# Performance work log

Measured on AMD Instinct MI355X. Metric: run time of the kernel, lower is better.

The kernel has to match this reference:

```python
import jax, jax.numpy as jnp
import numpy as np

N, H, P, NB, IN, E, B = 10000, 64, 12, 3, 3, 160000, 2
EPS = 1e-5


def _ln(x, w, b):
    # LayerNorm over last two dims [N, H] with affine params [N, H]
    mu = jnp.mean(x, axis=(-2, -1), keepdims=True)
    var = jnp.mean((x - mu) ** 2, axis=(-2, -1), keepdims=True)
    return (x - mu) * jax.lax.rsqrt(var + EPS) * w + b


def _proj(x, w1, b1, w2, b2):
    h = jax.nn.relu(jnp.einsum('...i,oi->...o', x, w1) + b1)
    return jnp.einsum('...i,oi->...o', h, w2) + b2


def setup_inputs() -> dict:
    key = jax.random.key(0)
    ks = jax.random.split(key, 24)
    s = lambda k, shape, fan: jax.random.normal(k, shape, jnp.float32) * (1.0 / np.sqrt(fan))
    inp = {
        'x': jax.random.normal(ks[0], (B, P, N, IN), jnp.float32),
        'edge_index': jax.random.randint(ks[1], (2, E), 0, N, jnp.int64),
        'pos': jax.random.normal(ks[2], (N, H), jnp.float32),
        # input projection (IN -> H -> H)
        'iw1': s(ks[3], (H, IN), IN), 'ib1': jnp.zeros((H,), jnp.float32),
        'iw2': s(ks[4], (H, H), H), 'ib2': jnp.zeros((H,), jnp.float32),
        # pos projection (H -> H -> H)
        'pw1': s(ks[5], (H, H), H), 'pb1': jnp.zeros((H,), jnp.float32),
        'pw2': s(ks[6], (H, H), H), 'pb2': jnp.zeros((H,), jnp.float32),
        # attention over skip connections [NB+1, 1]
        'attn': jax.random.normal(ks[7], (NB + 1, 1), jnp.float32),
        # per-block params, stacked on leading NB axis
        'gnw': jnp.ones((NB, N, H), jnp.float32), 'gnb': jnp.zeros((NB, N, H), jnp.float32),
        'tnw': jnp.ones((NB, N, H), jnp.float32), 'tnb': jnp.zeros((NB, N, H), jnp.float32),
        'tcw': s(ks[8], (NB, P, P), P), 'tcb': jnp.zeros((NB, P), jnp.float32),
        # output projection (H -> H -> H)
        'ow1': s(ks[9], (H, H), H), 'ob1': jnp.zeros((H,), jnp.float32),
        'ow2': s(ks[10], (H, H), H), 'ob2': jnp.zeros((H,), jnp.float32),
    }
    return inp


def reference(x, edge_index, pos, iw1, ib1, iw2, ib2, pw1, pb1, pw2, pb2,
              attn, gnw, gnb, tnw, tnb, tcw, tcb, ow1, ob1, ow2, ob2):
    row, col = edge_index[0], edge_index[1]
    # LGConv gcn_norm (no self loops): deg from target index, sym normalization
    deg = jax.ops.segment_sum(jnp.ones((E,), x.dtype), col, num_segments=N)
    dis = jnp.where(deg > 0, jax.lax.rsqrt(jnp.maximum(deg, 1.0)) * (deg > 0), 0.0)
    dis = jnp.where(deg > 0, deg ** -0.5, 0.0)
    norm = dis[row] * dis[col]  # [E]

    x = _proj(x, iw1, ib1, iw2, ib2)            # [B,P,N,H]
    x = x + _proj(pos, pw1, pb1, pw2, pb2)       # broadcast [N,H]

    skip = [x]
    for i in range(NB):
        x = _ln(x, gnw[i], gnb[i])
        # LightGCN propagate: out[col] += norm * x[row]
        msg = norm[:, None] * x[:, :, row, :]    # [B,P,E,H]
        x = jnp.zeros_like(x).at[:, :, col, :].add(msg)
        x = _ln(x, tnw[i], tnb[i])
        # 1x1 Conv2d over the period/channel axis
        x = jnp.einsum('qp,bpnh->bqnh', tcw[i], x) + tcb[i][None, :, None, None]
        skip.append(x)

    a = jax.nn.softmax(attn, axis=0)[:, 0]       # [NB+1]
    x = sum(s * a[k] for k, s in enumerate(skip))
    return _proj(x, ow1, ob1, ow2, ob2)
```

## Files before the change

### kernel.cpp

```cpp
#include <hip/hip_runtime.h>
#include <stdint.h>

constexpr int N_ = 10000, H_ = 64, P_ = 12, NB_ = 3, IN_ = 3, E_ = 160000, B_ = 2;
constexpr int S_  = B_ * P_;
constexpr int NH_ = N_ * H_;
constexpr int BPS_ = N_ / 4;
constexpr int NB64_ = (N_ + 63) / 64;
constexpr int NPAIR_ = S_ / 2;
constexpr int PROPNB_ = N_ / 8;
constexpr int PROPBLK_ = NPAIR_ * PROPNB_;
constexpr int PROPPX_  = PROPBLK_ / 8;
constexpr int EPAD_ = E_ + N_;
constexpr float EPS_ = 1e-5f;

#define DEVFN __device__ __forceinline__

DEVFN float softmax4(const float* a, int k) {
    float m = fmaxf(fmaxf(a[0], a[1]), fmaxf(a[2], a[3]));
    float e0 = __expf(a[0] - m), e1 = __expf(a[1] - m);
    float e2 = __expf(a[2] - m), e3 = __expf(a[3] - m);
    float s = e0 + e1 + e2 + e3;
    float ek = (k == 0 ? e0 : k == 1 ? e1 : k == 2 ? e2 : e3);
    return ek / s;
}

DEVFN float wred(float v) {
#pragma unroll
    for (int d = 32; d; d >>= 1) v += __shfl_xor(v, d, 64);
    return v;
}

DEVFN void fma4(float m, const float4& a, float4& acc) {
    acc.x = fmaf(m, a.x, acc.x); acc.y = fmaf(m, a.y, acc.y);
    acc.z = fmaf(m, a.z, acc.z); acc.w = fmaf(m, a.w, acc.w);
}

DEVFN void xred4(float4& a) {
    a.x += __shfl_xor(a.x, 16, 64); a.y += __shfl_xor(a.y, 16, 64);
    a.z += __shfl_xor(a.z, 16, 64); a.w += __shfl_xor(a.w, 16, 64);
    a.x += __shfl_xor(a.x, 32, 64); a.y += __shfl_xor(a.y, 32, 64);
    a.z += __shfl_xor(a.z, 32, 64); a.w += __shfl_xor(a.w, 32, 64);
}

DEVFN void stage_swz(const float4* __restrict__ src, float* __restrict__ dst, int t) {
    for (int f = t; f < 1024; f += 256) {
        int r = f >> 4, c4 = f & 15;
        float4 v = src[f];
        *(float4*)&dst[r * 64 + ((c4 ^ (r >> 2)) << 2)] = v;
    }
}

DEVFN void stage_swz_guard(const float4* __restrict__ src, float* __restrict__ dst,
                           int t, int nvalid) {
    for (int f = t; f < 1024; f += 256) {
        int r = f >> 4, c4 = f & 15;
        float4 v = make_float4(0.f, 0.f, 0.f, 0.f);
        if (r < nvalid) v = src[f];
        *(float4*)&dst[r * 64 + ((c4 ^ (r >> 2)) << 2)] = v;
    }
}

DEVFN void gemm64(const float* __restrict__ As, const float* __restrict__ Bs,
                  int tn4, int to4, float ov[4][4]) {
    const float* arow = As + tn4 * 64;
    const float* brow = Bs + to4 * 64;
#pragma unroll 4
    for (int j4 = 0; j4 < 16; ++j4) {
        int ca = (j4 << 2) ^ tn4;
        int cb = (j4 << 2) ^ to4;
        float4 a[4], b[4];
#pragma unroll
        for (int i = 0; i < 4; ++i) a[i] = *(const float4*)&arow[i * 64 + ca];
#pragma unroll
        for (int k = 0; k < 4; ++k) b[k] = *(const float4*)&brow[k * 64 + cb];
#pragma unroll
        for (int i = 0; i < 4; ++i)
#pragma unroll
            for (int k = 0; k < 4; ++k) {
                ov[i][k] = fmaf(a[i].x, b[k].x, ov[i][k]);
                ov[i][k] = fmaf(a[i].y, b[k].y, ov[i][k]);
                ov[i][k] = fmaf(a[i].z, b[k].z, ov[i][k]);
                ov[i][k] = fmaf(a[i].w, b[k].w, ov[i][k]);
            }
    }
}

__global__ void k_deg(const int* __restrict__ ei, int* __restrict__ deg) {
    int e = blockIdx.x * 256 + threadIdx.x;
    if (e < E_) atomicAdd(&deg[ei[E_ + e]], 1);
}

__global__ void k_scan(const int* __restrict__ deg, int* __restrict__ offs,
                       int* __restrict__ cursor, float* __restrict__ dis) {
    __shared__ int part[1024];
    int t = threadIdx.x;
    int base = t * 10;
    int cnt = 0;
    for (int k = 0; k < 10; k++) {
        int i = base + k;
        if (i < N_) cnt += (deg[i] + 1) & ~1;
    }
    part[t] = cnt;
    __syncthreads();
    for (int d = 1; d < 1024; d <<= 1) {
        int v = 0;
        if (t >= d) v = part[t - d];
        __syncthreads();
        if (t >= d) part[t] += v;
        __syncthreads();
    }
    int run = (t > 0) ? part[t - 1] : 0;
    for (int k = 0; k < 10; k++) {
        int i = base + k;
        if (i < N_) {
            offs[i] = run; cursor[i] = run;
            int dg = deg[i];
            dis[i] = dg > 0 ? rsqrtf((float)dg) : 0.f;
            run += (dg + 1) & ~1;
        }
    }
    if (t == 1023) offs[N_] = part[1023];
}

__global__ void k_scatter(const int* __restrict__ ei, const float* __restrict__ dis,
                          int* __restrict__ cursor, int2* __restrict__ csr_pack) {
    int e = blockIdx.x * 256 + threadIdx.x;
    if (e >= E_) return;
    int r = ei[e], c = ei[E_ + e];
    float nm = dis[r] * dis[c];
    int p = atomicAdd(&cursor[c], 1);
    csr_pack[p] = make_int2(r << 4, __float_as_int(nm));
}

__global__ void k_red(const float2* __restrict__ part, float* __restrict__ st, int count) {
    __shared__ float rsm[4], rsq[4];
    int s = blockIdx.x, t = threadIdx.x, w = t >> 6, lane = t & 63;
    float sm = 0.f, sq = 0.f;
    for (int k = t; k < count; k += 256) {
        float2 p = part[s * BPS_ + k];
        sm += p.x; sq += p.y;
    }
    sm = wred(sm); sq = wred(sq);
    if (lane == 0) { rsm[w] = sm; rsq[w] = sq; }
    __syncthreads();
    if (t == 0) {
        st[s * 2]     = rsm[0] + rsm[1] + rsm[2] + rsm[3];
        st[s * 2 + 1] = rsq[0] + rsq[1] + rsq[2] + rsq[3];
    }
}

__global__ void k_wb(const int* __restrict__ offs, const int2* __restrict__ csr_pack,
                     const float* __restrict__ gw, const float* __restrict__ gb,
                     float* __restrict__ Wt, float* __restrict__ Bt) {
    int t = threadIdx.x;
    int w = t >> 6, lane = t & 63;
    int sub = lane >> 4, hl = lane & 15;
    int n = blockIdx.x * 4 + w;
    const float4* W4 = (const float4*)gw;
    const float4* B4 = (const float4*)gb;
    int e0 = offs[n], e1 = offs[n + 1];
    float4 AW = make_float4(0, 0, 0, 0), AB = make_float4(0, 0, 0, 0);
    for (int e = e0 + sub * 2; e < e1; e += 8) {
        int4 mp = *(const int4*)&csr_pack[e];
        float m0 = __int_as_float(mp.y), m1 = __int_as_float(mp.w);
        int i0 = mp.x + hl, i1 = mp.z + hl;
        float4 a = W4[i0], b = W4[i1], c = B4[i0], d = B4[i1];
        fma4(m0, a, AW); fma4(m1, b, AW);
        fma4(m0, c, AB); fma4(m1, d, AB);
    }
    xred4(AW); xred4(AB);
    if (sub == 0) {
        ((float4*)Wt)[n * 16 + hl] = AW;
        ((float4*)Bt)[n * 16 + hl] = AB;
    }
}

__global__ void k_posproj(const float* __restrict__ pos, const float* __restrict__ w1,
                          const float* __restrict__ b1, const float* __restrict__ w2,
                          const float* __restrict__ b2, float* __restrict__ out) {
    __shared__ float w1T[64 * 65], w2T[64 * 65];
    __shared__ float stage[4][64];
    int t = threadIdx.x;
    for (int k = t; k < 4096; k += 256) {
        int o = k >> 6, j = k & 63;
        w1T[j * 65 + o] = w1[k];
        w2T[j * 65 + o] = w2[k];
    }
    __syncthreads();
    int w = t >> 6, lane = t & 63;
    int n = blockIdx.x * 4 + w;
    float v = pos[n * 64 + lane];
    stage[w][lane] = v;
    float h = b1[lane];
#pragma unroll
    for (int j = 0; j < 64; j++) h = fmaf(w1T[j * 65 + lane], stage[w][j], h);
    h = fmaxf(h, 0.f);
    stage[w][lane] = h;
    float o2 = b2[lane];
#pragma unroll
    for (int j = 0; j < 64; j++) o2 = fmaf(w2T[j * 65 + lane], stage[w][j], o2);
    out[n * 64 + lane] = o2;
}

__global__ void k_in(const float* __restrict__ xin, const float* __restrict__ iw1,
                     const float* __restrict__ ib1, const float* __restrict__ iw2,
                     const float* __restrict__ ib2, const float* __restrict__ pp,
                     const float* __restrict__ attn, const float* __restrict__ gw0,
                     float* __restrict__ xw, float* __restrict__ acc,
                     float2* __restrict__ part) {
    __shared__ __align__(16) float U[4096];
    __shared__ __align__(16) float B2s[4096];
    __shared__ float xin_s[192], iw1_s[192], bias1[64], bias2[64];
    __shared__ float rsm[4], rsq[4], sa0s;
    int t = threadIdx.x;
    int blk = blockIdx.x;
    int s = blk / NB64_, bn = blk % NB64_;
    int n0 = bn * 64;
    int nvalid = min(64, N_ - n0);
    stage_swz((const float4*)iw2, B2s, t);
    if (t < 192) {
        iw1_s[t] = iw1[t];
        int n = n0 + t / 3;
        xin_s[t] = (n < N_) ? xin[(size_t)s * (N_ * 3) + n0 * 3 + t] : 0.f;
    }
    if (t < 64) { bias1[t] = ib1[t]; bias2[t] = ib2[t]; }
    if (t == 0) sa0s = softmax4(attn, 0);
    __syncthreads();
    int tn = t >> 4, to = t & 15;
    int tn4 = tn << 2, to4 = to << 2;
    float h1[4][4];
#pragma unroll
    for (int i = 0; i < 4; i++) {
        float a0 = xin_s[(tn4 + i) * 3], a1 = xin_s[(tn4 + i) * 3 + 1],
              a2 = xin_s[(tn4 + i) * 3 + 2];
#pragma unroll
        for (int k = 0; k < 4; k++) {
            int o = to4 + k;
            float h = bias1[o];
            h = fmaf(iw1_s[o * 3], a0, h);
            h = fmaf(iw1_s[o * 3 + 1], a1, h);
            h = fmaf(iw1_s[o * 3 + 2], a2, h);
            h1[i][k] = fmaxf(h, 0.f);
        }
    }
#pragma unroll
    for (int i = 0; i < 4; i++)
        *(float4*)&U[(tn4 + i) * 64 + (to4 ^ tn4)] =
            make_float4(h1[i][0], h1[i][1], h1[i][2], h1[i][3]);
    __syncthreads();
    float ov[4][4];
#pragma unroll
    for (int i = 0; i < 4; i++)
#pragma unroll
        for (int k = 0; k < 4; k++) ov[i][k] = bias2[to4 + k];
    gemm64(U, B2s, tn4, to4, ov);
    __syncthreads();
#pragma unroll
    for (int i = 0; i < 4; i++)
        *(float4*)&U[(tn4 + i) * 64 + to4] =
            make_float4(ov[i][0], ov[i][1], ov[i][2], ov[i][3]);
    __syncthreads();
    const float4* pp4 = (const float4*)pp + n0 * 16;
    const float4* gw4 = (const float4*)gw0 + n0 * 16;
    float4* xw4 = (float4*)xw + (size_t)s * (NH_ / 4) + n0 * 16;
    float4* ac4 = (float4*)acc + (size_t)s * (NH_ / 4) + n0 * 16;
    float sa0 = sa0s;
    float sm = 0.f, sq = 0.f;
    for (int f = t; f < 1024; f += 256) {
        int r = f >> 4;
        if (r < nvalid) {
            float4 v = ((const float4*)U)[f];
            float4 p = pp4[f];
            v.x += p.x; v.y += p.y; v.z += p.z; v.w += p.w;
            float4 a;
            a.x = sa0 * v.x; a.y = sa0 * v.y; a.z = sa0 * v.z; a.w = sa0 * v.w;
            ac4[f] = a;
            sm += v.x + v.y + v.z + v.w;
            sq += v.x * v.x + v.y * v.y + v.z * v.z + v.w * v.w;
            float4 g = gw4[f];
            v.x *= g.x; v.y *= g.y; v.z *= g.z; v.w *= g.w;
            xw4[f] = v;
        }
    }
    int w = t >> 6, lane = t & 63;
    sm = wred(sm); sq = wred(sq);
    if (lane == 0) { rsm[w] = sm; rsq[w] = sq; }
    __syncthreads();
    if (t == 0) {
        float2 pr;
        pr.x = rsm[0] + rsm[1] + rsm[2] + rsm[3];
        pr.y = rsq[0] + rsq[1] + rsq[2] + rsq[3];
        part[s * BPS_ + bn] = pr;
    }
}

__global__ void k_prop(const float* __restrict__ xw, const int* __restrict__ offs,
                       const int2* __restrict__ csr_pack, const float* __restrict__ Wt,
                       const float* __restrict__ Bt, const float* __restrict__ st,
                       float* __restrict__ y, float2* __restrict__ part) {
    __shared__ float bs[4][2][4];
    int t = threadIdx.x;
    int w = t >> 6, lane = t & 63;
    int nsel = lane >> 5;
    int str  = (lane >> 4) & 1;
    int hl   = lane & 15;
    int orig = blockIdx.x;
    int gw = (orig & 7) * PROPPX_ + (orig >> 3);
    int pr = gw / PROPNB_;
    int blkin = gw % PROPNB_;
    int n = blkin * 8 + w * 2 + nsel;
    int s0 = pr * 2;
    const float4* xh0 = (const float4*)(xw + (size_t)s0 * NH_) + hl;
    const float4* xh1 = xh0 + (NH_ / 4);
    int e0 = offs[n], e1 = offs[n + 1];
    float4 A0 = make_float4(0, 0, 0, 0), A1 = make_float4(0, 0, 0, 0);
    int e = e0 + str * 2;
    while (__any(e < e1)) {
        if (e < e1) {
            int4 mp = *(const int4*)&csr_pack[e];
            float m0 = __int_as_float(mp.y), m1 = __int_as_float(mp.w);
            float4 a = xh0[mp.x], b = xh0[mp.z];
            float4 c = xh1[mp.x], d = xh1[mp.z];
            fma4(m0, a, A0); fma4(m1, b, A0);
            fma4(m0, c, A1); fma4(m1, d, A1);
        }
        e += 4;
    }
    A0.x += __shfl_xor(A0.x, 16, 64); A0.y += __shfl_xor(A0.y, 16, 64);
    A0.z += __shfl_xor(A0.z, 16, 64); A0.w += __shfl_xor(A0.w, 16, 64);
    A1.x += __shfl_xor(A1.x, 16, 64); A1.y += __shfl_xor(A1.y, 16, 64);
    A1.z += __shfl_xor(A1.z, 16, 64); A1.w += __shfl_xor(A1.w, 16, 64);
    float mu0 = st[s0 * 2] * (1.f / NH_);
    float v0  = st[s0 * 2 + 1] * (1.f / NH_) - mu0 * mu0;
    float rs0 = rsqrtf(v0 + EPS_);
    float mu1 = st[s0 * 2 + 2] * (1.f / NH_);
    float v1  = st[s0 * 2 + 3] * (1.f / NH_) - mu1 * mu1;
    float rs1 = rsqrtf(v1 + EPS_);
    float4 wt = ((const float4*)Wt)[n * 16 + hl];
    float4 bt = ((const float4*)Bt)[n * 16 + hl];
    float c0 = -mu0 * rs0, c1 = -mu1 * rs1;
    float4 y0, y1;
    y0.x = fmaf(rs0, A0.x, fmaf(c0, wt.x, bt.x));
    y0.y = fmaf(rs0, A0.y, fmaf(c0, wt.y, bt.y));
    y0.z = fmaf(rs0, A0.z, fmaf(c0, wt.z, bt.z));
    y0.w = fmaf(rs0, A0.w, fmaf(c0, wt.w, bt.w));
    y1.x = fmaf(rs1, A1.x, fmaf(c1, wt.x, bt.x));
    y1.y = fmaf(rs1, A1.y, fmaf(c1, wt.y, bt.y));
    y1.z = fmaf(rs1, A1.z, fmaf(c1, wt.z, bt.z));
    y1.w = fmaf(rs1, A1.w, fmaf(c1, wt.w, bt.w));
    if (str == 0) {
        float4* yp = (float4*)(y + (size_t)s0 * NH_ + (size_t)n * 64);
        yp[hl] = y0;
        yp[NH_ / 4 + hl] = y1;
    }
    float sum0 = y0.x + y0.y + y0.z + y0.w;
    float dot0 = fmaf(y0.x, y0.x, fmaf(y0.y, y0.y, fmaf(y0.z, y0.z, y0.w * y0.w)));
    float sum1 = y1.x + y1.y + y1.z + y1.w;
    float dot1 = fmaf(y1.x, y1.x, fmaf(y1.y, y1.y, fmaf(y1.z, y1.z, y1.w * y1.w)));
    float va = str ? dot0 : sum0;
    float vb = str ? dot1 : sum1;
#pragma unroll
    for (int d = 1; d <= 8; d <<= 1) {
        va += __shfl_xor(va, d, 64);
        vb += __shfl_xor(vb, d, 64);
    }
    if (hl == 0) {
        bs[w][nsel][str] = va;
        bs[w][nsel][2 + str] = vb;
    }
    __syncthreads();
    if (t < 2) {
        float psm = 0.f, psq = 0.f;
#pragma unroll
        for (int w2 = 0; w2 < 4; w2++)
#pragma unroll
            for (int ns = 0; ns < 2; ns++) {
                psm += bs[w2][ns][t * 2];
                psq += bs[w2][ns][t * 2 + 1];
            }
        part[(s0 + t) * BPS_ + blkin] = make_float2(psm, psq);
    }
}

__global__ void k_mix(const float* __restrict__ y, const float* __restrict__ tnw,
                      const float* __restrict__ tnb, const float* __restrict__ tcw,
                      const float* __restrict__ tcb, const float* __restrict__ st2,
                      const float* __restrict__ attn, int ai,
                      const float* __restrict__ wnext, int wx,
                      float* __restrict__ xn, float* __restrict__ acc,
                      float2* __restrict__ part) {
    __shared__ float smu[12], srs[12], scw[144], scb[12];
    __shared__ float sred[24][16];
    __shared__ float sa;
    int t = threadIdx.x;
    int gt = blockIdx.x * 256 + t;
    int b = gt / NH_, r = gt % NH_;
    if (t < 12) {
        int s = b * 12 + t;
        float mu = st2[s * 2] * (1.f / NH_);
        float var = st2[s * 2 + 1] * (1.f / NH_) - mu * mu;
        smu[t] = mu;
        srs[t] = rsqrtf(var + EPS_);
        scb[t] = tcb[t];
    }
    if (t < 144) scw[t] = tcw[t];
    if (t == 0) sa = softmax4(attn, ai);
    __syncthreads();
    float wv = tnw[r], bv = tnb[r];
    float wn = wx ? wnext[r] : 0.f;
    float yn[12];
#pragma unroll
    for (int p = 0; p < 12; p++) {
        float v = y[(size_t)(b * 12 + p) * NH_ + r];
        yn[p] = (v - smu[p]) * srs[p] * wv + bv;
    }
    float ov[12];
#pragma unroll
    for (int q = 0; q < 12; q++) {
        float o = scb[q];
#pragma unroll
        for (int p = 0; p < 12; p++) o = fmaf(scw[q * 12 + p], yn[p], o);
        ov[q] = o;
        size_t idx = (size_t)(b * 12 + q) * NH_ + r;
        if (wx) xn[idx] = o * wn;
        acc[idx] += sa * o;
    }
    int lane = t & 63;
    int w = t >> 6;
#pragma unroll
    for (int q = 0; q < 12; q++) {
        float sm = ov[q];
        float sq = ov[q] * ov[q];
#pragma unroll
        for (int d = 1; d <= 8; d <<= 1) {
            sm += __shfl_xor(sm, d, 64);
            sq += __shfl_xor(sq, d, 64);
        }
        if ((lane & 15) == 0) {
            int widx = (w << 2) | (lane >> 4);
            sred[q * 2][widx] = sm;
            sred[q * 2 + 1][widx] = sq;
        }
    }
    __syncthreads();
    if (t < 12) {
        float psm = 0.f, psq = 0.f;
#pragma unroll
        for (int k = 0; k < 16; k++) {
            psm += sred[t * 2][k];
            psq += sred[t * 2 + 1][k];
        }
        int jb = blockIdx.x % BPS_;
        part[(b * 12 + t) * BPS_ + jb] = make_float2(psm, psq);
    }
}

__global__ void k_out(float* __restrict__ io, const float* __restrict__ w1,
                      const float* __restrict__ b1, const float* __restrict__ w2,
                      const float* __restrict__ b2) {
    __shared__ __align__(16) float U[4096];
    __shared__ __align__(16) float B1s[4096], B2s[4096];
    __shared__ float bias1[64], bias2[64];
    int t = threadIdx.x;
    int blk = blockIdx.x;
    int s = blk / NB64_, bn = blk % NB64_;
    int n0 = bn * 64;
    int nvalid = min(64, N_ - n0);
    const float4* io4 = (const float4*)io + (size_t)s * (NH_ / 4) + n0 * 16;
    stage_swz((const float4*)w1, B1s, t);
    stage_swz((const float4*)w2, B2s, t);
    stage_swz_guard(io4, U, t, nvalid);
    if (t < 64) { bias1[t] = b1[t]; bias2[t] = b2[t]; }
    __syncthreads();
    int tn = t >> 4, to = t & 15;
    int tn4 = tn << 2, to4 = to << 2;
    float ov[4][4];
#pragma unroll
    for (int i = 0; i < 4; i++)
#pragma unroll
        for (int k = 0; k < 4; k++) ov[i][k] = bias1[to4 + k];
    gemm64(U, B1s, tn4, to4, ov);
#pragma unroll
    for (int i = 0; i < 4; i++)
#pragma unroll
        for (int k = 0; k < 4; k++) ov[i][k] = fmaxf(ov[i][k], 0.f);
    __syncthreads();
#pragma unroll
    for (int i = 0; i < 4; i++)
        *(float4*)&U[(tn4 + i) * 64 + (to4 ^ tn4)] =
            make_float4(ov[i][0], ov[i][1], ov[i][2], ov[i][3]);
    __syncthreads();
    float ov2[4][4];
#pragma unroll
    for (int i = 0; i < 4; i++)
#pragma unroll
        for (int k = 0; k < 4; k++) ov2[i][k] = bias2[to4 + k];
    gemm64(U, B2s, tn4, to4, ov2);
    __syncthreads();
#pragma unroll
    for (int i = 0; i < 4; i++)
        *(float4*)&U[(tn4 + i) * 64 + to4] =
            make_float4(ov2[i][0], ov2[i][1], ov2[i][2], ov2[i][3]);
    __syncthreads();
    float4* io4w = (float4*)io + (size_t)s * (NH_ / 4) + n0 * 16;
    for (int f = t; f < 1024; f += 256) {
        int r = f >> 4;
        if (r < nvalid) io4w[f] = ((const float4*)U)[f];
    }
}

extern "C" void kernel_launch(void* const* d_in, const int* in_sizes, int n_in,
                              void* d_out, int out_size, void* d_ws, size_t ws_size,
                              hipStream_t stream) {
    (void)in_sizes; (void)n_in; (void)out_size; (void)ws_size;
    const float* x    = (const float*)d_in[0];
    const int*   ei   = (const int*)d_in[1];
    const float* pos  = (const float*)d_in[2];
    const float* iw1  = (const float*)d_in[3];
    const float* ib1  = (const float*)d_in[4];
    const float* iw2  = (const float*)d_in[5];
    const float* ib2  = (const float*)d_in[6];
    const float* pw1  = (const float*)d_in[7];
    const float* pb1  = (const float*)d_in[8];
    const float* pw2  = (const float*)d_in[9];
    const float* pb2  = (const float*)d_in[10];
    const float* attn = (const float*)d_in[11];
    const float* gnw  = (const float*)d_in[12];
    const float* gnb  = (const float*)d_in[13];
    const float* tnw  = (const float*)d_in[14];
    const float* tnb  = (const float*)d_in[15];
    const float* tcw  = (const float*)d_in[16];
    const float* tcb  = (const float*)d_in[17];
    const float* ow1  = (const float*)d_in[18];
    const float* ob1  = (const float*)d_in[19];
    const float* ow2  = (const float*)d_in[20];
    const float* ob2  = (const float*)d_in[21];
    float* out = (float*)d_out;

    float* xA = (float*)d_ws;
    float* xB = xA + (size_t)S_ * NH_;
    float* yb = xB + (size_t)S_ * NH_;
    float* pp = yb + (size_t)S_ * NH_;
    float* Wt = pp + NH_;
    float* Bt = Wt + NH_;
    int2* csr_pack = (int2*)(Bt + NH_);
    int* deg     = (int*)(csr_pack + EPAD_);
    int* offs    = deg + N_;
    int* cursor  = offs + N_ + 1;
    float* dis   = (float*)(cursor + N_);
    float* st1   = dis + N_;
    float* st2   = st1 + 4 * S_ * 2;
    float2* partA = (float2*)(((uintptr_t)(st2 + 3 * S_ * 2) + 15) & ~(uintptr_t)15);

    hipMemsetAsync(csr_pack, 0, (size_t)EPAD_ * sizeof(int2) + N_ * sizeof(int), stream);

    k_deg<<<(E_ + 255) / 256, 256, 0, stream>>>(ei, deg);
    k_scan<<<1, 1024, 0, stream>>>(deg, offs, cursor, dis);
    k_scatter<<<(E_ + 255) / 256, 256, 0, stream>>>(ei, dis, cursor, csr_pack);
    k_posproj<<<N_ / 4, 256, 0, stream>>>(pos, pw1, pb1, pw2, pb2, pp);
    k_in<<<S_ * NB64_, 256, 0, stream>>>(x, iw1, ib1, iw2, ib2, pp, attn, gnw,
                                         xA, out, partA);
    k_red<<<S_, 256, 0, stream>>>(partA, st1 + 0 * S_ * 2, NB64_);

    float* cur = xA;
    float* nxt = xB;
    for (int i = 0; i < NB_; i++) {
        k_wb<<<N_ / 4, 256, 0, stream>>>(offs, csr_pack, gnw + (size_t)i * NH_,
                                         gnb + (size_t)i * NH_, Wt, Bt);
        k_prop<<<PROPBLK_, 256, 0, stream>>>(cur, offs, csr_pack, Wt, Bt,
                                             st1 + i * S_ * 2, yb, partA);
        k_red<<<S_, 256, 0, stream>>>(partA, st2 + i * S_ * 2, PROPNB_);
        int wx = (i < NB_ - 1) ? 1 : 0;
        const float* wnext = gnw + (size_t)(i + 1 < NB_ ? i + 1 : 0) * NH_;
        k_mix<<<B_ * NH_ / 256, 256, 0, stream>>>(yb, tnw + (size_t)i * NH_,
                                                  tnb + (size_t)i * NH_, tcw + i * 144,
                                                  tcb + i * 12, st2 + i * S_ * 2, attn, i + 1,
                                                  wnext, wx, nxt, out, partA);
        if (i < NB_ - 1)
            k_red<<<S_, 256, 0, stream>>>(partA, st1 + (i + 1) * S_ * 2, BPS_);
        float* tmp = cur; cur = nxt; nxt = tmp;
    }
    k_out<<<S_ * NB64_, 256, 0, stream>>>(out, ow1, ob1, ow2, ob2);
}
```

Baseline: 731.2 us.

## Remap propagation kernel to four nodes per wave, one slice each

The propagate kernel now gives each 16-lane group its own node within a single batch-period slice. Previously each wave handled two slices per node and split every node's edge list across two lane halves, which needed a shuffle to combine them. Each lane now walks the whole edge list with a 4-edge unrolled loop plus a remainder step, so the wave-wide `__any` loop and the cross-half reduction are gone. The cost is that edge metadata (`csr_pack`) is read once per slice instead of once per slice pair. Lanes within a wave also now have different trip counts because their nodes have different degrees.

```diff
diff --git a/kernel.cpp b/kernel.cpp
--- a/kernel.cpp
+++ b/kernel.cpp
@@ -6,9 +6,8 @@
 constexpr int NH_ = N_ * H_;
 constexpr int BPS_ = N_ / 4;
 constexpr int NB64_ = (N_ + 63) / 64;
-constexpr int NPAIR_ = S_ / 2;
-constexpr int PROPNB_ = N_ / 8;
-constexpr int PROPBLK_ = NPAIR_ * PROPNB_;
+constexpr int PROPNB_ = N_ / 16;
+constexpr int PROPBLK_ = S_ * PROPNB_;
 constexpr int PROPPX_  = PROPBLK_ / 8;
 constexpr int EPAD_ = E_ + N_;
 constexpr float EPS_ = 1e-5f;
@@ -298,87 +297,63 @@
                        const int2* __restrict__ csr_pack, const float* __restrict__ Wt,
                        const float* __restrict__ Bt, const float* __restrict__ st,
                        float* __restrict__ y, float2* __restrict__ part) {
-    __shared__ float bs[4][2][4];
+    __shared__ float2 bs[4][4];
     int t = threadIdx.x;
     int w = t >> 6, lane = t & 63;
-    int nsel = lane >> 5;
-    int str  = (lane >> 4) & 1;
-    int hl   = lane & 15;
+    int g = lane >> 4, hl = lane & 15;
     int orig = blockIdx.x;
     int gw = (orig & 7) * PROPPX_ + (orig >> 3);
-    int pr = gw / PROPNB_;
+    int s = gw / PROPNB_;
     int blkin = gw % PROPNB_;
-    int n = blkin * 8 + w * 2 + nsel;
-    int s0 = pr * 2;
-    const float4* xh0 = (const float4*)(xw + (size_t)s0 * NH_) + hl;
-    const float4* xh1 = xh0 + (NH_ / 4);
+    int n = blkin * 16 + w * 4 + g;
+    const float4* xh = (const float4*)(xw + (size_t)s * NH_) + hl;
     int e0 = offs[n], e1 = offs[n + 1];
-    float4 A0 = make_float4(0, 0, 0, 0), A1 = make_float4(0, 0, 0, 0);
-    int e = e0 + str * 2;
-    while (__any(e < e1)) {
-        if (e < e1) {
-            int4 mp = *(const int4*)&csr_pack[e];
-            float m0 = __int_as_float(mp.y), m1 = __int_as_float(mp.w);
-            float4 a = xh0[mp.x], b = xh0[mp.z];
-            float4 c = xh1[mp.x], d = xh1[mp.z];
-            fma4(m0, a, A0); fma4(m1, b, A0);
-            fma4(m0, c, A1); fma4(m1, d, A1);
-        }
-        e += 4;
-    }
-    A0.x += __shfl_xor(A0.x, 16, 64); A0.y += __shfl_xor(A0.y, 16, 64);
-    A0.z += __shfl_xor(A0.z, 16, 64); A0.w += __shfl_xor(A0.w, 16, 64);
-    A1.x += __shfl_xor(A1.x, 16, 64); A1.y += __shfl_xor(A1.y, 16, 64);
-    A1.z += __shfl_xor(A1.z, 16, 64); A1.w += __shfl_xor(A1.w, 16, 64);
-    float mu0 = st[s0 * 2] * (1.f / NH_);
-    float v0  = st[s0 * 2 + 1] * (1.f / NH_) - mu0 * mu0;
-    float rs0 = rsqrtf(v0 + EPS_);
-    float mu1 = st[s0 * 2 + 2] * (1.f / NH_);
-    float v1  = st[s0 * 2 + 3] * (1.f / NH_) - mu1 * mu1;
-    float rs1 = rsqrtf(v1 + EPS_);
+    float4 A = make_float4(0, 0, 0, 0);
+    int e = e0;
+    for (; e + 2 < e1; e += 4) {
+        int4 m0 = *(const int4*)&csr_pack[e];
+        int4 m1 = *(const int4*)&csr_pack[e + 2];
+        float4 a = xh[m0.x], b = xh[m0.z];
+        float4 c = xh[m1.x], d = xh[m1.z];
+        fma4(__int_as_float(m0.y), a, A); fma4(__int_as_float(m0.w), b, A);
+        fma4(__int_as_float(m1.y), c, A); fma4(__int_as_float(m1.w), d, A);
+    }
+    if (e < e1) {
+        int4 m0 = *(const int4*)&csr_pack[e];
+        float4 a = xh[m0.x], b = xh[m0.z];
+        fma4(__int_as_float(m0.y), a, A); fma4(__int_as_float(m0.w), b, A);
+    }
+    float mu = st[s * 2] * (1.f / NH_);
+    float va = st[s * 2 + 1] * (1.f / NH_) - mu * mu;
+    float rs = rsqrtf(va + EPS_);
+    float c0 = -mu * rs;
     float4 wt = ((const float4*)Wt)[n * 16 + hl];
     float4 bt = ((const float4*)Bt)[n * 16 + hl];
-    float c0 = -mu0 * rs0, c1 = -mu1 * rs1;
-    float4 y0, y1;
-    y0.x = fmaf(rs0, A0.x, fmaf(c0, wt.x, bt.x));
-    y0.y = fmaf(rs0, A0.y, fmaf(c0, wt.y, bt.y));
-    y0.z = fmaf(rs0, A0.z, fmaf(c0, wt.z, bt.z));
-    y0.w = fmaf(rs0, A0.w, fmaf(c0, wt.w, bt.w));
-    y1.x = fmaf(rs1, A1.x, fmaf(c1, wt.x, bt.x));
-    y1.y = fmaf(rs1, A1.y, fmaf(c1, wt.y, bt.y));
-    y1.z = fmaf(rs1, A1.z, fmaf(c1, wt.z, bt.z));
-    y1.w = fmaf(rs1, A1.w, fmaf(c1, wt.w, bt.w));
-    if (str == 0) {
-        float4* yp = (float4*)(y + (size_t)s0 * NH_ + (size_t)n * 64);
-        yp[hl] = y0;
-        yp[NH_ / 4 + hl] = y1;
-    }
-    float sum0 = y0.x + y0.y + y0.z + y0.w;
-    float dot0 = fmaf(y0.x, y0.x, fmaf(y0.y, y0.y, fmaf(y0.z, y0.z, y0.w * y0.w)));
-    float sum1 = y1.x + y1.y + y1.z + y1.w;
-    float dot1 = fmaf(y1.x, y1.x, fmaf(y1.y, y1.y, fmaf(y1.z, y1.z, y1.w * y1.w)));
-    float va = str ? dot0 : sum0;
-    float vb = str ? dot1 : sum1;
+    float4 y0;
+    y0.x = fmaf(rs, A.x, fmaf(c0, wt.x, bt.x));
+    y0.y = fmaf(rs, A.y, fmaf(c0, wt.y, bt.y));
+    y0.z = fmaf(rs, A.z, fmaf(c0, wt.z, bt.z));
+    y0.w = fmaf(rs, A.w, fmaf(c0, wt.w, bt.w));
+    ((float4*)(y + (size_t)s * NH_ + (size_t)n * 64))[hl] = y0;
+    float sm = y0.x + y0.y + y0.z + y0.w;
+    float sq = fmaf(y0.x, y0.x, fmaf(y0.y, y0.y, fmaf(y0.z, y0.z, y0.w * y0.w)));
 #pragma unroll
     for (int d = 1; d <= 8; d <<= 1) {
-        va += __shfl_xor(va, d, 64);
-        vb += __shfl_xor(vb, d, 64);
-    }
-    if (hl == 0) {
-        bs[w][nsel][str] = va;
-        bs[w][nsel][2 + str] = vb;
-    }
-    __syncthreads();
-    if (t < 2) {
+        sm += __shfl_xor(sm, d, 64);
+        sq += __shfl_xor(sq, d, 64);
+    }
+    if (hl == 0) bs[w][g] = make_float2(sm, sq);
+    __syncthreads();
+    if (t == 0) {
         float psm = 0.f, psq = 0.f;
 #pragma unroll
         for (int w2 = 0; w2 < 4; w2++)
 #pragma unroll
-            for (int ns = 0; ns < 2; ns++) {
-                psm += bs[w2][ns][t * 2];
-                psq += bs[w2][ns][t * 2 + 1];
+            for (int g2 = 0; g2 < 4; g2++) {
+                psm += bs[w2][g2].x;
+                psq += bs[w2][g2].y;
             }
-        part[(s0 + t) * BPS_ + blkin] = make_float2(psm, psq);
+        part[s * BPS_ + blkin] = make_float2(psm, psq);
     }
 }
 
```

Result: no change. 722.5 us (-1.2%).
